# Kernel tuning notes

Hardware: AMD Instinct MI355X
Metric: run time of the kernel (lower is better)

Reference implementation:

```python
import jax, jax.numpy as jnp
import numpy as np

B, T, D = 2, 2048, 2048
NH, NKV, HD = 16, 4, 128
ROPE_DIMS = 64
EPS = 1e-6


def _rope_tables(t, rd, base=10000.0):
    # rd dims are rotated as two halves of size rd//2; cos/sin are [T, rd]
    inv_freq = 1.0 / (base ** (jnp.arange(0, rd // 2, dtype=jnp.float32) * 2.0 / rd))
    ang = jnp.arange(t, dtype=jnp.float32)[:, None] * inv_freq[None, :]  # [T, rd//2]
    ang = jnp.concatenate([ang, ang], axis=-1)  # [T, rd]
    return jnp.cos(ang), jnp.sin(ang)


def setup_inputs() -> dict:
    key = jax.random.key(0)
    ks = jax.random.split(key, 6)
    x = jax.random.normal(ks[0], (B, T, D), dtype=jnp.float32)
    cos, sin = _rope_tables(T, ROPE_DIMS)
    s = 1.0 / np.sqrt(D)
    wq = jax.random.normal(ks[1], (NH * HD, D), dtype=jnp.float32) * s
    wk = jax.random.normal(ks[2], (NKV * HD, D), dtype=jnp.float32) * s
    wv = jax.random.normal(ks[3], (NKV * HD, D), dtype=jnp.float32) * s
    wo = jax.random.normal(ks[4], (NH * HD, D), dtype=jnp.float32).T * s  # [NH*HD, D] -> stored torch-style below
    wo = jax.random.normal(ks[5], (D, NH * HD), dtype=jnp.float32) * s  # torch Linear weight [out,in]
    w_norm = jnp.ones((D,), dtype=jnp.float32)
    return {"x": x, "cos": cos, "sin": sin, "w_norm": w_norm, "wq": wq,
            "wk": wk, "wv": wv, "wo": wo, "rope_dims": ROPE_DIMS, "use_xsa": 1}


def _rmsnorm(x, w, eps=EPS):
    ms = jnp.mean(x * x, axis=-1, keepdims=True)
    return x * jax.lax.rsqrt(ms + eps) * w


def _rotate_half(x):
    x1, x2 = jnp.split(x, 2, axis=-1)
    return jnp.concatenate([-x2, x1], axis=-1)


def _apply_partial_rope(q, k, cos, sin, rd):
    # q: [B,T,NH,HD], k: [B,T,NKV,HD]; cos/sin: [T,rd]
    c = cos[None, :, None, :]
    s = sin[None, :, None, :]
    def rot(t):
        tr, tp = t[..., :rd], t[..., rd:]
        tr = tr * c + _rotate_half(tr) * s
        return jnp.concatenate([tr, tp], axis=-1)
    return rot(q), rot(k)


def reference(x, cos, sin, w_norm, wq, wk, wv, wo, rope_dims, use_xsa):
    b, t, d = x.shape
    group = NH // NKV
    h = _rmsnorm(x, w_norm)
    q = jnp.einsum('btd,ed->bte', h, wq).reshape(b, t, NH, HD)
    k = jnp.einsum('btd,ed->bte', h, wk).reshape(b, t, NKV, HD)
    v = jnp.einsum('btd,ed->bte', h, wv).reshape(b, t, NKV, HD)
    q, k = _apply_partial_rope(q, k, cos, sin, rope_dims)
    # GQA: repeat KV heads across groups, then [B,H,T,HD]
    k = jnp.repeat(k, group, axis=2).transpose(0, 2, 1, 3)
    v = jnp.repeat(v, group, axis=2).transpose(0, 2, 1, 3)
    q = q.transpose(0, 2, 1, 3)
    scores = jnp.einsum('bhqd,bhkd->bhqk', q, k) / np.sqrt(HD)
    causal = jnp.tril(jnp.ones((t, t), dtype=bool))
    scores = jnp.where(causal[None, None], scores, jnp.finfo(scores.dtype).min)
    attn = jax.nn.softmax(scores, axis=-1)
    out = jnp.einsum('bhqk,bhkd->bhqd', attn, v)
    if use_xsa:
        dot = jnp.sum(out * v, axis=-1, keepdims=True)
        vns = jnp.sum(v * v, axis=-1, keepdims=True) + 1e-6
        out = out - dot * v / vns
    out = out.transpose(0, 2, 1, 3).reshape(b, t, NH * HD)
    return jnp.einsum('bte,de->btd', out, wo)
```

## Files before the change

kernel.cpp:

```cpp
#include <hip/hip_runtime.h>
#include <hip/hip_bf16.h>
#include <stdint.h>

#define B_ 2
#define T_ 2048
#define D_ 2048
#define NH_ 16
#define NKV_ 4
#define HD_ 128
#define EQ_ (NH_*HD_)
#define EKV_ (NKV_*HD_)
#define EQKV_ (EQ_ + 2*EKV_)
#define KOFF_ EQ_
#define VOFF_ (EQ_ + EKV_)

typedef __attribute__((ext_vector_type(8))) short short8;
typedef __attribute__((ext_vector_type(4))) short short4x;
typedef __attribute__((ext_vector_type(4))) float floatx4;
typedef __attribute__((ext_vector_type(4))) uint uintx4;

static __device__ __forceinline__ ushort f2bf(float f) {
  uint u = __builtin_bit_cast(uint, f);
  u = (u + 0x7fffu + ((u >> 16) & 1u)) >> 16;
  return (ushort)u;
}
static __device__ __forceinline__ float bf2f(ushort u) {
  return __builtin_bit_cast(float, ((uint)u) << 16);
}
static __device__ __forceinline__ uint cvt_pk_bf16(float lo, float hi) {
  uint r;
  asm("v_cvt_pk_bf16_f32 %0, %1, %2" : "=v"(r) : "v"(lo), "v"(hi));
  return r;
}

#define S1_ (EQ_*D_)
#define S2_ (S1_ + EKV_*D_)
#define S3_ (S2_ + EKV_*D_)
#define S4_ (S3_ + D_*EQ_)
__global__ __launch_bounds__(256) void cvt4_k(const float* __restrict__ wq,
                                              const float* __restrict__ wk,
                                              const float* __restrict__ wv,
                                              const float* __restrict__ wo,
                                              ushort* __restrict__ wqkv,
                                              ushort* __restrict__ wob) {
  int i = (blockIdx.x * 256 + threadIdx.x) * 2;
  const float* s;
  ushort* d;
  int j;
  if (i < S1_)      { s = wq; d = wqkv + i; j = i; }
  else if (i < S2_) { s = wk; d = wqkv + i; j = i - S1_; }
  else if (i < S3_) { s = wv; d = wqkv + i; j = i - S2_; }
  else              { s = wo; d = wob + (i - S3_); j = i - S3_; }
  float2 f = *(const float2*)&s[j];
  ushort2 u;
  u.x = f2bf(f.x);
  u.y = f2bf(f.y);
  *(ushort2*)d = u;
}

__global__ __launch_bounds__(256) void rmsnorm_k(const float* __restrict__ x,
                                                 const float* __restrict__ wn,
                                                 ushort* __restrict__ hb) {
  const int row = blockIdx.x, tid = threadIdx.x;
  const int w = tid >> 6, lane = tid & 63;
  const float* xr = x + (size_t)row * D_;
  float v[8];
  float4 a = *(const float4*)&xr[tid * 8];
  float4 b = *(const float4*)&xr[tid * 8 + 4];
  v[0] = a.x; v[1] = a.y; v[2] = a.z; v[3] = a.w;
  v[4] = b.x; v[5] = b.y; v[6] = b.z; v[7] = b.w;
  float ss = 0.f;
#pragma unroll
  for (int i = 0; i < 8; i++) ss += v[i] * v[i];
  for (int m = 32; m; m >>= 1) ss += __shfl_xor(ss, m);
  __shared__ float red[4];
  if (lane == 0) red[w] = ss;
  __syncthreads();
  float tot = red[0] + red[1] + red[2] + red[3];
  float sc = rsqrtf(tot * (1.f / D_) + 1e-6f);
  short8 st;
#pragma unroll
  for (int i = 0; i < 8; i++) st[i] = (short)f2bf(v[i] * sc * wn[tid * 8 + i]);
  *(short8*)(hb + (size_t)row * D_ + tid * 8) = st;
}

template <bool OUT_F32>
__global__ __launch_bounds__(256) void gemm_bt(const ushort* __restrict__ A,
                                               const ushort* __restrict__ W,
                                               void* __restrict__ Cp,
                                               int M, int N, int K) {
  __shared__ __align__(16) ushort lA[128 * 64];
  __shared__ __align__(16) ushort lB[128 * 64];
  const int tid = threadIdx.x;
  const int w = tid >> 6, lane = tid & 63;
  const int bm = blockIdx.y, bn = blockIdx.x;
  const int wm = w >> 1, wn = w & 1;
  const int l15 = lane & 15, l4 = lane >> 4;
  const int swz = (l15 & 7) * 8;

  floatx4 acc[4][4];
#pragma unroll
  for (int m = 0; m < 4; m++)
#pragma unroll
    for (int n = 0; n < 4; n++) acc[m][n] = floatx4{0.f, 0.f, 0.f, 0.f};

  for (int k0 = 0; k0 < K; k0 += 64) {
#pragma unroll
    for (int r = 0; r < 4; ++r) {
      int c = r * 256 + tid;
      int row = c >> 3, cw = c & 7;
      int scol = k0 + ((cw ^ (row & 7)) << 3);
      const ushort* ga = A + (size_t)(bm * 128 + row) * K + scol;
      __builtin_amdgcn_global_load_lds(
          (const __attribute__((address_space(1))) void*)ga,
          (__attribute__((address_space(3))) void*)&lA[c * 8], 16, 0, 0);
      const ushort* gb = W + (size_t)(bn * 128 + row) * K + scol;
      __builtin_amdgcn_global_load_lds(
          (const __attribute__((address_space(1))) void*)gb,
          (__attribute__((address_space(3))) void*)&lB[c * 8], 16, 0, 0);
    }
    __syncthreads();
#pragma unroll
    for (int kk = 0; kk < 2; kk++) {
      short8 av[4], bv[4];
      int co = (kk * 32 + l4 * 8) ^ swz;
#pragma unroll
      for (int m = 0; m < 4; m++)
        av[m] = *(const short8*)&lA[(wm * 64 + m * 16 + l15) * 64 + co];
#pragma unroll
      for (int n = 0; n < 4; n++)
        bv[n] = *(const short8*)&lB[(wn * 64 + n * 16 + l15) * 64 + co];
#pragma unroll
      for (int m = 0; m < 4; m++)
#pragma unroll
        for (int n = 0; n < 4; n++)
          acc[m][n] = __builtin_amdgcn_mfma_f32_16x16x32_bf16(av[m], bv[n], acc[m][n], 0, 0, 0);
    }
    __syncthreads();
  }

  if (OUT_F32) {
    float* C = (float*)Cp;
#pragma unroll
    for (int m = 0; m < 4; m++)
#pragma unroll
      for (int n = 0; n < 4; n++)
#pragma unroll
        for (int j = 0; j < 4; j++) {
          int row = bm * 128 + wm * 64 + m * 16 + l4 * 4 + j;
          int col = bn * 128 + wn * 64 + n * 16 + l15;
          C[(size_t)row * N + col] = acc[m][n][j];
        }
  } else {
    ushort* C = (ushort*)Cp;
#pragma unroll
    for (int m = 0; m < 4; m++)
#pragma unroll
      for (int n = 0; n < 4; n++)
#pragma unroll
        for (int j = 0; j < 4; j++) {
          int row = bm * 128 + wm * 64 + m * 16 + l4 * 4 + j;
          int col = bn * 128 + wn * 64 + n * 16 + l15;
          C[(size_t)row * N + col] = f2bf(acc[m][n][j]);
        }
  }
}

__global__ __launch_bounds__(256) void rope_k(ushort* __restrict__ X,
                                              const float* __restrict__ cosT,
                                              const float* __restrict__ sinT,
                                              int rd) {
  int idx = blockIdx.x * 256 + threadIdx.x;
  int half = rd >> 1;
  int total = B_ * T_ * (NH_ + NKV_) * half;
  if (idx >= total) return;
  int i = idx % half;
  int r2 = idx / half;
  int hh = r2 % (NH_ + NKV_);
  int row = r2 / (NH_ + NKV_);
  int t = row % T_;
  int col = (hh < NH_) ? hh * HD_ : KOFF_ + (hh - NH_) * HD_;
  ushort* p = X + (size_t)row * EQKV_ + col;
  float x0 = bf2f(p[i]), x1 = bf2f(p[i + half]);
  float c0 = cosT[t * rd + i], s0 = sinT[t * rd + i];
  float c1 = cosT[t * rd + i + half], s1 = sinT[t * rd + i + half];
  p[i] = f2bf(x0 * c0 - x1 * s0);
  p[i + half] = f2bf(x1 * c1 + x0 * s1);
}

__global__ __launch_bounds__(256) void vtr_k(const ushort* __restrict__ V,
                                             int vstride,
                                             ushort* __restrict__ Vt) {
  __shared__ ushort tile[32][34];
  const int tb = blockIdx.x, eb = blockIdx.y, b = blockIdx.z;
  const int tid = threadIdx.x;
  const int r = tid >> 3, c4 = (tid & 7) * 4;
  short4x in = *(const short4x*)&V[((size_t)(b * T_ + tb * 32 + r)) * vstride + eb * 32 + c4];
#pragma unroll
  for (int i = 0; i < 4; i++) tile[r][c4 + i] = (ushort)in[i];
  __syncthreads();
  short4x out;
#pragma unroll
  for (int i = 0; i < 4; i++) out[i] = (short)tile[c4 + i][r];
  *(short4x*)&Vt[((size_t)(b * EKV_ + eb * 32 + r)) * T_ + tb * 32 + c4] = out;
}

__global__ __launch_bounds__(256, 2) void attn_k(const ushort* __restrict__ QKV,
                                                 const ushort* __restrict__ Vt,
                                                 const int* __restrict__ flag,
                                                 ushort* __restrict__ att) {
  __shared__ __align__(16) ushort Klds[2][8192];
  __shared__ __align__(16) ushort Vlds[2][8192];
  const int tid = threadIdx.x, w = tid >> 6, lane = tid & 63;
  const int l15 = lane & 15, l4 = lane >> 4;
  const int alpha = lane >> 5;
  const int srcA = ((lane >> 4) & 1) * 32 + l15;
  const int srcB = srcA + 16;
  const int h = blockIdx.y, b = blockIdx.z, kv = h >> 2;
  const int px = blockIdx.x;
  const float c_ = 0.12752626f;
  const float THR_ = 90.5f;
  const int flagv = *flag;

  const ushort* Kh = QKV + KOFF_ + (size_t)b * T_ * EQKV_ + kv * HD_;
  const ushort* Vth = Vt + ((size_t)(b * EKV_ + kv * HD_)) * T_;

  auto stageK = [&](int buf, const ushort* kp) {
#pragma unroll
    for (int i = 0; i < 4; i++) {
      int q = i * 256 + tid;
      int r = q >> 4, cw = q & 15;
      const ushort* src = kp + (size_t)r * EQKV_ + ((cw ^ (r & 7)) << 3);
      __builtin_amdgcn_global_load_lds(
          (const __attribute__((address_space(1))) void*)src,
          (__attribute__((address_space(3))) void*)&Klds[buf][q * 8], 16, 0, 0);
    }
  };
  auto stageV = [&](int buf, const ushort* vp) {
#pragma unroll
    for (int i = 0; i < 4; i++) {
      int q = i * 256 + tid;
      int d = q >> 3, cw = q & 7;
      const ushort* src = vp + (size_t)d * T_ + ((cw ^ (d & 7)) << 3);
      __builtin_amdgcn_global_load_lds(
          (const __attribute__((address_space(1))) void*)src,
          (__attribute__((address_space(3))) void*)&Vlds[buf][q * 8], 16, 0, 0);
    }
  };

  for (int hh = 0; hh < 2; hh++) {
    const int qb = hh ? (31 - px) : px;
    const int nt = qb + 1;
    const int qbase = qb * 64 + w * 16;
    const int myq = qbase + l15;

    short8 qf[4];
#pragma unroll
    for (int kk = 0; kk < 4; kk++)
      qf[kk] = *(const short8*)&QKV[(size_t)(b * T_ + qbase + l15) * EQKV_ + h * HD_ + kk * 32 + l4 * 8];

    floatx4 acc_o[8];
#pragma unroll
    for (int nn = 0; nn < 8; nn++) acc_o[nn] = floatx4{0.f, 0.f, 0.f, 0.f};
    float m_ = -1e30f;
    float l_ = 0.f;

    const ushort* kp = Kh;
    const ushort* vp = Vth;
    stageV(0, vp);
    stageK(0, kp);
    __syncthreads();
    int cur = 0;

    for (int t = 0; t < nt; t++) {
      const int kvb = t * 64;
      if (t + 1 < nt) {
        stageV(cur ^ 1, vp + 64);
        stageK(cur ^ 1, kp + 64 * EQKV_);
      }
      kp += 64 * EQKV_;
      vp += 64;

      floatx4 s[4];
#pragma unroll
      for (int n = 0; n < 4; n++) s[n] = floatx4{0.f, 0.f, 0.f, 0.f};
      __builtin_amdgcn_s_setprio(1);
#pragma unroll
      for (int n = 0; n < 4; n++) {
        int row = n * 16 + l15;
#pragma unroll
        for (int kk = 0; kk < 4; kk++) {
          int bc = (kk * 64 + l4 * 16) ^ ((row & 7) << 4);
          short8 kf = *(const short8*)&Klds[cur][row * 128 + (bc >> 1)];
          s[n] = __builtin_amdgcn_mfma_f32_16x16x32_bf16(kf, qf[kk], s[n], 0, 0, 0);
        }
      }
      __builtin_amdgcn_s_setprio(0);

      float pm = -1e30f;
      if (t == nt - 1) {
#pragma unroll
        for (int n = 0; n < 4; n++)
#pragma unroll
          for (int j = 0; j < 4; j++) {
            int k = kvb + n * 16 + l4 * 4 + j;
            float sv = (k <= myq) ? s[n][j] : -1e30f;
            s[n][j] = sv;
            pm = fmaxf(pm, sv);
          }
      } else {
#pragma unroll
        for (int n = 0; n < 4; n++)
#pragma unroll
          for (int j = 0; j < 4; j++) pm = fmaxf(pm, s[n][j]);
      }
      pm = fmaxf(pm, __shfl_xor(pm, 16));
      pm = fmaxf(pm, __shfl_xor(pm, 32));

      if (!__all(pm - m_ <= THR_)) {
        float mn = fmaxf(m_, pm);
        float f = exp2f((m_ - mn) * c_);
        m_ = mn;
        l_ *= f;
        float fj0 = __shfl(f, l4 * 4 + 0);
        float fj1 = __shfl(f, l4 * 4 + 1);
        float fj2 = __shfl(f, l4 * 4 + 2);
        float fj3 = __shfl(f, l4 * 4 + 3);
#pragma unroll
        for (int nn = 0; nn < 8; nn++) {
          acc_o[nn][0] *= fj0;
          acc_o[nn][1] *= fj1;
          acc_o[nn][2] *= fj2;
          acc_o[nn][3] *= fj3;
        }
      }

      float mc = m_ * c_;
      float ps = 0.f;
      float p_[4][4];
#pragma unroll
      for (int n = 0; n < 4; n++)
#pragma unroll
        for (int j = 0; j < 4; j++) {
          float p = exp2f(__builtin_fmaf(s[n][j], c_, -mc));
          p_[n][j] = p;
          ps += p;
        }
      ps += __shfl_xor(ps, 16);
      ps += __shfl_xor(ps, 32);
      l_ += ps;
      uint pk01[4], pk23[4];
#pragma unroll
      for (int n = 0; n < 4; n++) {
        pk01[n] = cvt_pk_bf16(p_[n][0], p_[n][1]);
        pk23[n] = cvt_pk_bf16(p_[n][2], p_[n][3]);
      }

      __builtin_amdgcn_s_setprio(1);
#pragma unroll
      for (int kk = 0; kk < 2; kk++) {
        int a01_0 = __shfl((int)pk01[2 * kk + 0], srcA);
        int a01_1 = __shfl((int)pk01[2 * kk + 1], srcA);
        int a23_0 = __shfl((int)pk23[2 * kk + 0], srcA);
        int a23_1 = __shfl((int)pk23[2 * kk + 1], srcA);
        int b01_0 = __shfl((int)pk01[2 * kk + 0], srcB);
        int b01_1 = __shfl((int)pk01[2 * kk + 1], srcB);
        int b23_0 = __shfl((int)pk23[2 * kk + 0], srcB);
        int b23_1 = __shfl((int)pk23[2 * kk + 1], srcB);
        uintx4 du;
        du.x = (uint)(alpha ? a01_1 : a01_0);
        du.y = (uint)(alpha ? a23_1 : a23_0);
        du.z = (uint)(alpha ? b01_1 : b01_0);
        du.w = (uint)(alpha ? b23_1 : b23_0);
        short8 pa = __builtin_bit_cast(short8, du);
#pragma unroll
        for (int n = 0; n < 8; n++) {
          int d = n * 16 + l15;
          int bc = (kk * 64 + l4 * 16) ^ ((d & 7) << 4);
          short8 vf = *(const short8*)&Vlds[cur][d * 64 + (bc >> 1)];
          acc_o[n] = __builtin_amdgcn_mfma_f32_16x16x32_bf16(pa, vf, acc_o[n], 0, 0, 0);
        }
      }
      __builtin_amdgcn_s_setprio(0);
      __syncthreads();
      cur ^= 1;
    }

    float inv_ = 1.f / l_;
#pragma unroll
    for (int j = 0; j < 4; j++) {
      float inv = __shfl(inv_, l4 * 4 + j);
      int q = qbase + l4 * 4 + j;
      const ushort* vq = QKV + VOFF_ + (size_t)(b * T_ + q) * EQKV_ + kv * HD_;
      float ov[8], vv[8], dot = 0.f, vns = 0.f;
#pragma unroll
      for (int n = 0; n < 8; n++) {
        float o = acc_o[n][j] * inv;
        float v = bf2f(vq[n * 16 + l15]);
        ov[n] = o;
        vv[n] = v;
        dot += o * v;
        vns += v * v;
      }
      dot += __shfl_xor(dot, 1); vns += __shfl_xor(vns, 1);
      dot += __shfl_xor(dot, 2); vns += __shfl_xor(vns, 2);
      dot += __shfl_xor(dot, 4); vns += __shfl_xor(vns, 4);
      dot += __shfl_xor(dot, 8); vns += __shfl_xor(vns, 8);
      if (flagv) {
        float f = dot / (vns + 1e-6f);
#pragma unroll
        for (int n = 0; n < 8; n++) ov[n] -= f * vv[n];
      }
      ushort* ap = att + (size_t)(b * T_ + q) * EQ_ + h * HD_;
#pragma unroll
      for (int n = 0; n < 8; n++) ap[n * 16 + l15] = f2bf(ov[n]);
    }
  }
}

extern "C" void kernel_launch(void* const* d_in, const int* in_sizes, int n_in,
                              void* d_out, int out_size, void* d_ws, size_t ws_size,
                              hipStream_t stream) {
  const float* x    = (const float*)d_in[0];
  const float* cosT = (const float*)d_in[1];
  const float* sinT = (const float*)d_in[2];
  const float* wn   = (const float*)d_in[3];
  const float* wq   = (const float*)d_in[4];
  const float* wk   = (const float*)d_in[5];
  const float* wv   = (const float*)d_in[6];
  const float* wo   = (const float*)d_in[7];
  const int* use_xsa = (const int*)d_in[9];
  int rd = in_sizes[1] / T_;

  char* ws = (char*)d_ws;
  size_t off = 0;
  auto alloc = [&](size_t bytes) {
    char* p = ws + off;
    off += (bytes + 255) & ~(size_t)255;
    return p;
  };
  ushort* h_b    = (ushort*)alloc((size_t)B_ * T_ * D_ * 2);
  ushort* qkv_b  = (ushort*)alloc((size_t)B_ * T_ * EQKV_ * 2);
  ushort* wqkv_b = (ushort*)alloc((size_t)EQKV_ * D_ * 2);
  ushort* wo_b   = (ushort*)alloc((size_t)D_ * EQ_ * 2);
  ushort* att_b  = h_b;
  ushort* vt_b   = wqkv_b;

  cvt4_k<<<S4_ / 512, 256, 0, stream>>>(wq, wk, wv, wo, wqkv_b, wo_b);
  rmsnorm_k<<<B_ * T_, 256, 0, stream>>>(x, wn, h_b);

  dim3 gqkv(EQKV_ / 128, B_ * T_ / 128);
  gemm_bt<false><<<gqkv, 256, 0, stream>>>(h_b, wqkv_b, qkv_b, B_ * T_, EQKV_, D_);

  dim3 gvt(T_ / 32, EKV_ / 32, B_);
  vtr_k<<<gvt, 256, 0, stream>>>(qkv_b + VOFF_, EQKV_, vt_b);

  int half = rd / 2;
  int tot = B_ * T_ * (NH_ + NKV_) * half;
  rope_k<<<(tot + 255) / 256, 256, 0, stream>>>(qkv_b, cosT, sinT, rd);

  dim3 ga(16, NH_, B_);
  attn_k<<<ga, 256, 0, stream>>>(qkv_b, vt_b, use_xsa, att_b);

  dim3 go(D_ / 128, B_ * T_ / 128);
  gemm_bt<true><<<go, 256, 0, stream>>>(att_b, wo_b, d_out, B_ * T_, D_, D_);
}
```

Measured before the change: 211.9 us.

## Pre-pack K/V into MFMA fragment layout and read directly from global in attention

Replaces the V transpose kernel with two packing kernels that write K and V tiles in the exact per-lane MFMA fragment order. The attention kernel then loads fragments straight from global/L2 with one contiguous 16-byte read per lane, so it no longer needs LDS staging, double buffering or barriers. The grid is also remapped so each wave owns an independent 16-row query tile, with the longest tiles launched first, replacing the paired-block causal balancing. This trades LDS reuse across waves for global/L2 traffic and adds an extra packing launch, and it drops the occupancy hint of 2 blocks per CU.

```diff
diff --git a/kernel.cpp b/kernel.cpp
--- a/kernel.cpp
+++ b/kernel.cpp
@@ -15,7 +15,6 @@
 #define VOFF_ (EQ_ + EKV_)
 
 typedef __attribute__((ext_vector_type(8))) short short8;
-typedef __attribute__((ext_vector_type(4))) short short4x;
 typedef __attribute__((ext_vector_type(4))) float floatx4;
 typedef __attribute__((ext_vector_type(4))) uint uintx4;
 
@@ -188,233 +187,215 @@
   p[i + half] = f2bf(x1 * c1 + x0 * s1);
 }
 
-__global__ __launch_bounds__(256) void vtr_k(const ushort* __restrict__ V,
-                                             int vstride,
-                                             ushort* __restrict__ Vt) {
-  __shared__ ushort tile[32][34];
-  const int tb = blockIdx.x, eb = blockIdx.y, b = blockIdx.z;
+__global__ __launch_bounds__(256) void kpack_k(const ushort* __restrict__ qkv,
+                                               ushort* __restrict__ kp) {
+  const int tile = blockIdx.x, kvh = blockIdx.y, b = blockIdx.z;
   const int tid = threadIdx.x;
-  const int r = tid >> 3, c4 = (tid & 7) * 4;
-  short4x in = *(const short4x*)&V[((size_t)(b * T_ + tb * 32 + r)) * vstride + eb * 32 + c4];
-#pragma unroll
-  for (int i = 0; i < 4; i++) tile[r][c4 + i] = (ushort)in[i];
+  const ushort* src0 = qkv + (size_t)(b * T_ + tile * 64) * EQKV_ + KOFF_ + kvh * HD_;
+  ushort* dst0 = kp + (((size_t)(b * NKV_ + kvh) * 32 + tile) * 8192);
+#pragma unroll
+  for (int i = 0; i < 4; i++) {
+    int q = i * 256 + tid;
+    int r = q >> 4, c8 = q & 15;
+    int n = r >> 4, l15 = r & 15, kk = c8 >> 2, l4 = c8 & 3;
+    short8 v = *(const short8*)&src0[(size_t)r * EQKV_ + c8 * 8];
+    *(short8*)&dst0[(((n * 4 + kk) * 64) + l4 * 16 + l15) * 8] = v;
+  }
+}
+
+__global__ __launch_bounds__(256) void vpack_k(const ushort* __restrict__ qkv,
+                                               ushort* __restrict__ vp) {
+  __shared__ ushort vt_[64][136];
+  const int tile = blockIdx.x, kvh = blockIdx.y, b = blockIdx.z;
+  const int tid = threadIdx.x;
+  const ushort* src0 = qkv + (size_t)(b * T_ + tile * 64) * EQKV_ + VOFF_ + kvh * HD_;
+  ushort* dst0 = vp + (((size_t)(b * NKV_ + kvh) * 32 + tile) * 8192);
+#pragma unroll
+  for (int i = 0; i < 4; i++) {
+    int q = i * 256 + tid;
+    int r = q >> 4, c8 = q & 15;
+    *(short8*)&vt_[r][c8 * 8] = *(const short8*)&src0[(size_t)r * EQKV_ + c8 * 8];
+  }
   __syncthreads();
-  short4x out;
-#pragma unroll
-  for (int i = 0; i < 4; i++) out[i] = (short)tile[c4 + i][r];
-  *(short4x*)&Vt[((size_t)(b * EKV_ + eb * 32 + r)) * T_ + tb * 32 + c4] = out;
-}
-
-__global__ __launch_bounds__(256, 2) void attn_k(const ushort* __restrict__ QKV,
-                                                 const ushort* __restrict__ Vt,
-                                                 const int* __restrict__ flag,
-                                                 ushort* __restrict__ att) {
-  __shared__ __align__(16) ushort Klds[2][8192];
-  __shared__ __align__(16) ushort Vlds[2][8192];
+#pragma unroll
+  for (int i = 0; i < 4; i++) {
+    int q = i * 256 + tid;
+    int frag = q >> 6, lane = q & 63;
+    int kk = frag >> 3, n = frag & 7;
+    int l4 = lane >> 4, l15 = lane & 15;
+    int d = n * 16 + l15, tl = kk * 32 + l4 * 8;
+    short8 o;
+#pragma unroll
+    for (int j = 0; j < 8; j++) o[j] = (short)vt_[tl + j][d];
+    *(short8*)&dst0[q * 8] = o;
+  }
+}
+
+__global__ __launch_bounds__(256) void attn_k(const ushort* __restrict__ QKV,
+                                              const ushort* __restrict__ kp,
+                                              const ushort* __restrict__ vp,
+                                              const int* __restrict__ flag,
+                                              ushort* __restrict__ att) {
   const int tid = threadIdx.x, w = tid >> 6, lane = tid & 63;
   const int l15 = lane & 15, l4 = lane >> 4;
   const int alpha = lane >> 5;
   const int srcA = ((lane >> 4) & 1) * 32 + l15;
   const int srcB = srcA + 16;
   const int h = blockIdx.y, b = blockIdx.z, kv = h >> 2;
-  const int px = blockIdx.x;
   const float c_ = 0.12752626f;
   const float THR_ = 90.5f;
   const int flagv = *flag;
 
-  const ushort* Kh = QKV + KOFF_ + (size_t)b * T_ * EQKV_ + kv * HD_;
-  const ushort* Vth = Vt + ((size_t)(b * EKV_ + kv * HD_)) * T_;
-
-  auto stageK = [&](int buf, const ushort* kp) {
-#pragma unroll
-    for (int i = 0; i < 4; i++) {
-      int q = i * 256 + tid;
-      int r = q >> 4, cw = q & 15;
-      const ushort* src = kp + (size_t)r * EQKV_ + ((cw ^ (r & 7)) << 3);
-      __builtin_amdgcn_global_load_lds(
-          (const __attribute__((address_space(1))) void*)src,
-          (__attribute__((address_space(3))) void*)&Klds[buf][q * 8], 16, 0, 0);
-    }
-  };
-  auto stageV = [&](int buf, const ushort* vp) {
-#pragma unroll
-    for (int i = 0; i < 4; i++) {
-      int q = i * 256 + tid;
-      int d = q >> 3, cw = q & 7;
-      const ushort* src = vp + (size_t)d * T_ + ((cw ^ (d & 7)) << 3);
-      __builtin_amdgcn_global_load_lds(
-          (const __attribute__((address_space(1))) void*)src,
-          (__attribute__((address_space(3))) void*)&Vlds[buf][q * 8], 16, 0, 0);
-    }
-  };
-
-  for (int hh = 0; hh < 2; hh++) {
-    const int qb = hh ? (31 - px) : px;
-    const int nt = qb + 1;
-    const int qbase = qb * 64 + w * 16;
-    const int myq = qbase + l15;
-
-    short8 qf[4];
-#pragma unroll
-    for (int kk = 0; kk < 4; kk++)
-      qf[kk] = *(const short8*)&QKV[(size_t)(b * T_ + qbase + l15) * EQKV_ + h * HD_ + kk * 32 + l4 * 8];
-
-    floatx4 acc_o[8];
-#pragma unroll
-    for (int nn = 0; nn < 8; nn++) acc_o[nn] = floatx4{0.f, 0.f, 0.f, 0.f};
-    float m_ = -1e30f;
-    float l_ = 0.f;
-
-    const ushort* kp = Kh;
-    const ushort* vp = Vth;
-    stageV(0, vp);
-    stageK(0, kp);
-    __syncthreads();
-    int cur = 0;
-
-    for (int t = 0; t < nt; t++) {
-      const int kvb = t * 64;
-      if (t + 1 < nt) {
-        stageV(cur ^ 1, vp + 64);
-        stageK(cur ^ 1, kp + 64 * EQKV_);
+  const int qt = (31 - blockIdx.x) * 4 + w;
+  const int nt = (qt >> 2) + 1;
+  const int qbase = qt * 16;
+  const int myq = qbase + l15;
+
+  const ushort* Kt0 = kp + ((size_t)(b * NKV_ + kv) * 32) * 8192;
+  const ushort* Vt0 = vp + ((size_t)(b * NKV_ + kv) * 32) * 8192;
+
+  short8 qf[4];
+#pragma unroll
+  for (int kk = 0; kk < 4; kk++)
+    qf[kk] = *(const short8*)&QKV[(size_t)(b * T_ + qbase + l15) * EQKV_ + h * HD_ + kk * 32 + l4 * 8];
+
+  floatx4 acc_o[8];
+#pragma unroll
+  for (int nn = 0; nn < 8; nn++) acc_o[nn] = floatx4{0.f, 0.f, 0.f, 0.f};
+  float m_ = -1e30f;
+  float l_ = 0.f;
+
+  for (int t = 0; t < nt; t++) {
+    const ushort* Kt = Kt0 + (size_t)t * 8192;
+    const ushort* Vt = Vt0 + (size_t)t * 8192;
+
+    floatx4 s[4];
+#pragma unroll
+    for (int n = 0; n < 4; n++) s[n] = floatx4{0.f, 0.f, 0.f, 0.f};
+    __builtin_amdgcn_s_setprio(1);
+#pragma unroll
+    for (int n = 0; n < 4; n++) {
+#pragma unroll
+      for (int kk = 0; kk < 4; kk++) {
+        short8 kf = *(const short8*)&Kt[((n * 4 + kk) * 64 + lane) * 8];
+        s[n] = __builtin_amdgcn_mfma_f32_16x16x32_bf16(kf, qf[kk], s[n], 0, 0, 0);
       }
-      kp += 64 * EQKV_;
-      vp += 64;
-
-      floatx4 s[4];
-#pragma unroll
-      for (int n = 0; n < 4; n++) s[n] = floatx4{0.f, 0.f, 0.f, 0.f};
-      __builtin_amdgcn_s_setprio(1);
-#pragma unroll
-      for (int n = 0; n < 4; n++) {
-        int row = n * 16 + l15;
-#pragma unroll
-        for (int kk = 0; kk < 4; kk++) {
-          int bc = (kk * 64 + l4 * 16) ^ ((row & 7) << 4);
-          short8 kf = *(const short8*)&Klds[cur][row * 128 + (bc >> 1)];
-          s[n] = __builtin_amdgcn_mfma_f32_16x16x32_bf16(kf, qf[kk], s[n], 0, 0, 0);
+    }
+    __builtin_amdgcn_s_setprio(0);
+
+    float pm = -1e30f;
+    if (t == nt - 1) {
+#pragma unroll
+      for (int n = 0; n < 4; n++)
+#pragma unroll
+        for (int j = 0; j < 4; j++) {
+          int k = t * 64 + n * 16 + l4 * 4 + j;
+          float sv = (k <= myq) ? s[n][j] : -1e30f;
+          s[n][j] = sv;
+          pm = fmaxf(pm, sv);
         }
+    } else {
+#pragma unroll
+      for (int n = 0; n < 4; n++)
+#pragma unroll
+        for (int j = 0; j < 4; j++) pm = fmaxf(pm, s[n][j]);
+    }
+    pm = fmaxf(pm, __shfl_xor(pm, 16));
+    pm = fmaxf(pm, __shfl_xor(pm, 32));
+
+    if (!__all(pm - m_ <= THR_)) {
+      float mn = fmaxf(m_, pm);
+      float f = exp2f((m_ - mn) * c_);
+      m_ = mn;
+      l_ *= f;
+      float fj0 = __shfl(f, l4 * 4 + 0);
+      float fj1 = __shfl(f, l4 * 4 + 1);
+      float fj2 = __shfl(f, l4 * 4 + 2);
+      float fj3 = __shfl(f, l4 * 4 + 3);
+#pragma unroll
+      for (int nn = 0; nn < 8; nn++) {
+        acc_o[nn][0] *= fj0;
+        acc_o[nn][1] *= fj1;
+        acc_o[nn][2] *= fj2;
+        acc_o[nn][3] *= fj3;
       }
-      __builtin_amdgcn_s_setprio(0);
-
-      float pm = -1e30f;
-      if (t == nt - 1) {
-#pragma unroll
-        for (int n = 0; n < 4; n++)
-#pragma unroll
-          for (int j = 0; j < 4; j++) {
-            int k = kvb + n * 16 + l4 * 4 + j;
-            float sv = (k <= myq) ? s[n][j] : -1e30f;
-            s[n][j] = sv;
-            pm = fmaxf(pm, sv);
-          }
-      } else {
-#pragma unroll
-        for (int n = 0; n < 4; n++)
-#pragma unroll
-          for (int j = 0; j < 4; j++) pm = fmaxf(pm, s[n][j]);
+    }
+
+    float mc = m_ * c_;
+    float ps = 0.f;
+    float p_[4][4];
+#pragma unroll
+    for (int n = 0; n < 4; n++)
+#pragma unroll
+      for (int j = 0; j < 4; j++) {
+        float p = exp2f(__builtin_fmaf(s[n][j], c_, -mc));
+        p_[n][j] = p;
+        ps += p;
       }
-      pm = fmaxf(pm, __shfl_xor(pm, 16));
-      pm = fmaxf(pm, __shfl_xor(pm, 32));
-
-      if (!__all(pm - m_ <= THR_)) {
-        float mn = fmaxf(m_, pm);
-        float f = exp2f((m_ - mn) * c_);
-        m_ = mn;
-        l_ *= f;
-        float fj0 = __shfl(f, l4 * 4 + 0);
-        float fj1 = __shfl(f, l4 * 4 + 1);
-        float fj2 = __shfl(f, l4 * 4 + 2);
-        float fj3 = __shfl(f, l4 * 4 + 3);
-#pragma unroll
-        for (int nn = 0; nn < 8; nn++) {
-          acc_o[nn][0] *= fj0;
-          acc_o[nn][1] *= fj1;
-          acc_o[nn][2] *= fj2;
-          acc_o[nn][3] *= fj3;
-        }
+    ps += __shfl_xor(ps, 16);
+    ps += __shfl_xor(ps, 32);
+    l_ += ps;
+    uint pk01[4], pk23[4];
+#pragma unroll
+    for (int n = 0; n < 4; n++) {
+      pk01[n] = cvt_pk_bf16(p_[n][0], p_[n][1]);
+      pk23[n] = cvt_pk_bf16(p_[n][2], p_[n][3]);
+    }
+
+    __builtin_amdgcn_s_setprio(1);
+#pragma unroll
+    for (int kk = 0; kk < 2; kk++) {
+      int a01_0 = __shfl((int)pk01[2 * kk + 0], srcA);
+      int a01_1 = __shfl((int)pk01[2 * kk + 1], srcA);
+      int a23_0 = __shfl((int)pk23[2 * kk + 0], srcA);
+      int a23_1 = __shfl((int)pk23[2 * kk + 1], srcA);
+      int b01_0 = __shfl((int)pk01[2 * kk + 0], srcB);
+      int b01_1 = __shfl((int)pk01[2 * kk + 1], srcB);
+      int b23_0 = __shfl((int)pk23[2 * kk + 0], srcB);
+      int b23_1 = __shfl((int)pk23[2 * kk + 1], srcB);
+      uintx4 du;
+      du.x = (uint)(alpha ? a01_1 : a01_0);
+      du.y = (uint)(alpha ? a23_1 : a23_0);
+      du.z = (uint)(alpha ? b01_1 : b01_0);
+      du.w = (uint)(alpha ? b23_1 : b23_0);
+      short8 pa = __builtin_bit_cast(short8, du);
+#pragma unroll
+      for (int n = 0; n < 8; n++) {
+        short8 vf = *(const short8*)&Vt[((kk * 8 + n) * 64 + lane) * 8];
+        acc_o[n] = __builtin_amdgcn_mfma_f32_16x16x32_bf16(pa, vf, acc_o[n], 0, 0, 0);
       }
-
-      float mc = m_ * c_;
-      float ps = 0.f;
-      float p_[4][4];
-#pragma unroll
-      for (int n = 0; n < 4; n++)
-#pragma unroll
-        for (int j = 0; j < 4; j++) {
-          float p = exp2f(__builtin_fmaf(s[n][j], c_, -mc));
-          p_[n][j] = p;
-          ps += p;
-        }
-      ps += __shfl_xor(ps, 16);
-      ps += __shfl_xor(ps, 32);
-      l_ += ps;
-      uint pk01[4], pk23[4];
-#pragma unroll
-      for (int n = 0; n < 4; n++) {
-        pk01[n] = cvt_pk_bf16(p_[n][0], p_[n][1]);
-        pk23[n] = cvt_pk_bf16(p_[n][2], p_[n][3]);
-      }
-
-      __builtin_amdgcn_s_setprio(1);
-#pragma unroll
-      for (int kk = 0; kk < 2; kk++) {
-        int a01_0 = __shfl((int)pk01[2 * kk + 0], srcA);
-        int a01_1 = __shfl((int)pk01[2 * kk + 1], srcA);
-        int a23_0 = __shfl((int)pk23[2 * kk + 0], srcA);
-        int a23_1 = __shfl((int)pk23[2 * kk + 1], srcA);
-        int b01_0 = __shfl((int)pk01[2 * kk + 0], srcB);
-        int b01_1 = __shfl((int)pk01[2 * kk + 1], srcB);
-        int b23_0 = __shfl((int)pk23[2 * kk + 0], srcB);
-        int b23_1 = __shfl((int)pk23[2 * kk + 1], srcB);
-        uintx4 du;
-        du.x = (uint)(alpha ? a01_1 : a01_0);
-        du.y = (uint)(alpha ? a23_1 : a23_0);
-        du.z = (uint)(alpha ? b01_1 : b01_0);
-        du.w = (uint)(alpha ? b23_1 : b23_0);
-        short8 pa = __builtin_bit_cast(short8, du);
-#pragma unroll
-        for (int n = 0; n < 8; n++) {
-          int d = n * 16 + l15;
-          int bc = (kk * 64 + l4 * 16) ^ ((d & 7) << 4);
-          short8 vf = *(const short8*)&Vlds[cur][d * 64 + (bc >> 1)];
-          acc_o[n] = __builtin_amdgcn_mfma_f32_16x16x32_bf16(pa, vf, acc_o[n], 0, 0, 0);
-        }
-      }
-      __builtin_amdgcn_s_setprio(0);
-      __syncthreads();
-      cur ^= 1;
-    }
-
-    float inv_ = 1.f / l_;
-#pragma unroll
-    for (int j = 0; j < 4; j++) {
-      float inv = __shfl(inv_, l4 * 4 + j);
-      int q = qbase + l4 * 4 + j;
-      const ushort* vq = QKV + VOFF_ + (size_t)(b * T_ + q) * EQKV_ + kv * HD_;
-      float ov[8], vv[8], dot = 0.f, vns = 0.f;
-#pragma unroll
-      for (int n = 0; n < 8; n++) {
-        float o = acc_o[n][j] * inv;
-        float v = bf2f(vq[n * 16 + l15]);
-        ov[n] = o;
-        vv[n] = v;
-        dot += o * v;
-        vns += v * v;
-      }
-      dot += __shfl_xor(dot, 1); vns += __shfl_xor(vns, 1);
-      dot += __shfl_xor(dot, 2); vns += __shfl_xor(vns, 2);
-      dot += __shfl_xor(dot, 4); vns += __shfl_xor(vns, 4);
-      dot += __shfl_xor(dot, 8); vns += __shfl_xor(vns, 8);
-      if (flagv) {
-        float f = dot / (vns + 1e-6f);
-#pragma unroll
-        for (int n = 0; n < 8; n++) ov[n] -= f * vv[n];
-      }
-      ushort* ap = att + (size_t)(b * T_ + q) * EQ_ + h * HD_;
-#pragma unroll
-      for (int n = 0; n < 8; n++) ap[n * 16 + l15] = f2bf(ov[n]);
-    }
+    }
+    __builtin_amdgcn_s_setprio(0);
+  }
+
+  float inv_ = 1.f / l_;
+#pragma unroll
+  for (int j = 0; j < 4; j++) {
+    float inv = __shfl(inv_, l4 * 4 + j);
+    int q = qbase + l4 * 4 + j;
+    const ushort* vq = QKV + VOFF_ + (size_t)(b * T_ + q) * EQKV_ + kv * HD_;
+    float ov[8], vv[8], dot = 0.f, vns = 0.f;
+#pragma unroll
+    for (int n = 0; n < 8; n++) {
+      float o = acc_o[n][j] * inv;
+      float v = bf2f(vq[n * 16 + l15]);
+      ov[n] = o;
+      vv[n] = v;
+      dot += o * v;
+      vns += v * v;
+    }
+    dot += __shfl_xor(dot, 1); vns += __shfl_xor(vns, 1);
+    dot += __shfl_xor(dot, 2); vns += __shfl_xor(vns, 2);
+    dot += __shfl_xor(dot, 4); vns += __shfl_xor(vns, 4);
+    dot += __shfl_xor(dot, 8); vns += __shfl_xor(vns, 8);
+    if (flagv) {
+      float f = dot / (vns + 1e-6f);
+#pragma unroll
+      for (int n = 0; n < 8; n++) ov[n] -= f * vv[n];
+    }
+    ushort* ap = att + (size_t)(b * T_ + q) * EQ_ + h * HD_;
+#pragma unroll
+    for (int n = 0; n < 8; n++) ap[n * 16 + l15] = f2bf(ov[n]);
   }
 }
 
@@ -444,23 +425,25 @@
   ushort* wqkv_b = (ushort*)alloc((size_t)EQKV_ * D_ * 2);
   ushort* wo_b   = (ushort*)alloc((size_t)D_ * EQ_ * 2);
   ushort* att_b  = h_b;
-  ushort* vt_b   = wqkv_b;
+  ushort* kp_b   = wqkv_b;
+  ushort* vp_b   = wqkv_b + (size_t)B_ * NKV_ * 32 * 8192;
 
   cvt4_k<<<S4_ / 512, 256, 0, stream>>>(wq, wk, wv, wo, wqkv_b, wo_b);
   rmsnorm_k<<<B_ * T_, 256, 0, stream>>>(x, wn, h_b);
 
   dim3 gqkv(EQKV_ / 128, B_ * T_ / 128);
   gemm_bt<false><<<gqkv, 256, 0, stream>>>(h_b, wqkv_b, qkv_b, B_ * T_, EQKV_, D_);
-
-  dim3 gvt(T_ / 32, EKV_ / 32, B_);
-  vtr_k<<<gvt, 256, 0, stream>>>(qkv_b + VOFF_, EQKV_, vt_b);
 
   int half = rd / 2;
   int tot = B_ * T_ * (NH_ + NKV_) * half;
   rope_k<<<(tot + 255) / 256, 256, 0, stream>>>(qkv_b, cosT, sinT, rd);
 
-  dim3 ga(16, NH_, B_);
-  attn_k<<<ga, 256, 0, stream>>>(qkv_b, vt_b, use_xsa, att_b);
+  dim3 gp(T_ / 64, NKV_, B_);
+  kpack_k<<<gp, 256, 0, stream>>>(qkv_b, kp_b);
+  vpack_k<<<gp, 256, 0, stream>>>(qkv_b, vp_b);
+
+  dim3 ga(32, NH_, B_);
+  attn_k<<<ga, 256, 0, stream>>>(qkv_b, kp_b, vp_b, use_xsa, att_b);
 
   dim3 go(D_ / 128, B_ * T_ / 128);
   gemm_bt<true><<<go, 256, 0, stream>>>(att_b, wo_b, d_out, B_ * T_, D_, D_);
```

New measurement: 539.7 us. 155% more time.
